# Kernel optimization log

Measured on AMD Instinct MI355X. Metric: run time of the kernel, lower is better.

## Reference

```python
import jax, jax.numpy as jnp
import numpy as np

V, E, H, D_IMG, A = 32000, 512, 512, 2048, 128
PAD_ID = 0
LN_EPS = 1e-5


def setup_inputs() -> dict:
    key = jax.random.key(0)
    ks = jax.random.split(key, 20)
    B, S, T = 32, 49, 64
    s = 0.02
    embed = jax.random.normal(ks[0], (V, E), jnp.float32) * s
    embed = embed.at[PAD_ID].set(0.0)
    return {
        "img_seq": jax.random.normal(ks[1], (B, S, D_IMG), jnp.float32),
        "tokens_in": jax.random.randint(ks[2], (B, T), 0, V, jnp.int64),
        "embed": embed,
        "W_ctx": jax.random.normal(ks[3], (E, D_IMG), jnp.float32) * s,
        "W_mix": jax.random.normal(ks[4], (E, 2 * E), jnp.float32) * s,
        "ln_g": jnp.ones((E,), jnp.float32),
        "ln_b": jnp.zeros((E,), jnp.float32),
        "W_ih": jax.random.normal(ks[5], (4 * H, E), jnp.float32) * s,
        "W_hh": jax.random.normal(ks[6], (4 * H, H), jnp.float32) * s,
        "b_ih": jnp.zeros((4 * H,), jnp.float32),
        "b_hh": jnp.zeros((4 * H,), jnp.float32),
        "W_head": jax.random.normal(ks[7], (V, H), jnp.float32) * s,
        "W_img": jax.random.normal(ks[8], (A, D_IMG), jnp.float32) * s,
        "W_hid": jax.random.normal(ks[9], (A, H), jnp.float32) * s,
        "w_score": jax.random.normal(ks[10], (A,), jnp.float32) * s,
        "W_h0": jax.random.normal(ks[11], (H, D_IMG), jnp.float32) * s,
        "b_h0": jnp.zeros((H,), jnp.float32),
        "W_c0": jax.random.normal(ks[12], (H, D_IMG), jnp.float32) * s,
        "b_c0": jnp.zeros((H,), jnp.float32),
    }


def _decode(img_seq, tokens_in, embed, W_ctx, W_mix, ln_g, ln_b,
            W_ih, W_hh, b_ih, b_hh, W_head, W_img, W_hid, w_score,
            W_h0, b_h0, W_c0, b_c0):
    # precompute image projection: [B,S,A]
    proj_image = jnp.einsum('bsd,ad->bsa', img_seq, W_img)
    g = img_seq.mean(1)  # [B, D_img]
    h = jnp.tanh(g @ W_h0.T + b_h0) * 0.5
    c = jnp.tanh(g @ W_c0.T + b_c0) * 0.5

    def step(carry, tok_t):
        h, c = carry
        emb = embed[tok_t] * (tok_t != PAD_ID)[:, None].astype(embed.dtype)
        # additive attention
        ph = h @ W_hid.T  # [B,A]
        comb = jnp.tanh(proj_image + ph[:, None, :])  # [B,S,A]
        scores = jnp.einsum('bsa,a->bs', comb, w_score)
        w = jax.nn.softmax(scores, axis=-1)
        ctx = jnp.einsum('bs,bsd->bd', w, img_seq)
        ctxE = ctx @ W_ctx.T
        x = jnp.concatenate([emb, ctxE], axis=-1) @ W_mix.T
        x = jax.nn.relu(x)
        mu = x.mean(-1, keepdims=True)
        var = ((x - mu) ** 2).mean(-1, keepdims=True)
        x = (x - mu) * jax.lax.rsqrt(var + LN_EPS) * ln_g + ln_b
        x = x + emb
        # LSTMCell (torch gate order: i, f, g, o)
        gates = x @ W_ih.T + b_ih + h @ W_hh.T + b_hh
        i_, f_, g_, o_ = jnp.split(gates, 4, axis=-1)
        c2 = jax.nn.sigmoid(f_) * c + jax.nn.sigmoid(i_) * jnp.tanh(g_)
        h2 = jax.nn.sigmoid(o_) * jnp.tanh(c2)
        logits = h2 @ W_head.T
        return (h2, c2), logits

    _, outs = jax.lax.scan(step, (h, c), tokens_in.T)  # [T,B,V]
    return jnp.transpose(outs, (1, 0, 2))  # [B,T,V]


def reference(img_seq, tokens_in, embed, W_ctx, W_mix, ln_g, ln_b,
              W_ih, W_hh, b_ih, b_hh, W_head, W_img, W_hid, w_score,
              W_h0, b_h0, W_c0, b_c0):
    return _decode(img_seq, tokens_in, embed, W_ctx, W_mix, ln_g, ln_b,
                   W_ih, W_hh, b_ih, b_hh, W_head, W_img, W_hid, w_score,
                   W_h0, b_h0, W_c0, b_c0)
```

## Files before the change

### kernel.cpp

```cpp
#include <hip/hip_runtime.h>

#define NV 32000
#define NT 64
#define NBLK 256u

typedef unsigned long long ull;
typedef unsigned short ushort;
typedef __attribute__((ext_vector_type(8))) short v8s;
typedef __attribute__((ext_vector_type(4))) float v4f;

#define WS_WBF     0
#define WS_H2BF    8192000
#define WS_IMGEM   8716288
#define WS_PROJ    9568256
#define WS_EMBM    9781248
#define WS_WHHBF   10829824
#define WS_WIHBF   11354112
#define WS_WHIDBF  11878400
#define WS_H       11911168
#define WS_XN      11943936
#define WS_C       11960320
#define WS_FLAGS   11976704
#define WS_G       11979264
#define PS_IMGBF   0
#define PS_WCTXBF  1703936
#define PS_WIMGBF  2228224
#define PS_WMIXRBF 2359296
#define PS_WMIXLBF 2490368
#define PS_IMGEBF  3342336

__device__ __forceinline__ float fsig(float x) {
    x = fminf(fmaxf(x, -30.f), 30.f);
    return 1.f / (1.f + __expf(-x));
}
__device__ __forceinline__ float ftanh(float x) {
    x = fminf(fmaxf(x, -15.f), 15.f);
    float e = __expf(2.f * x);
    return (e - 1.f) / (e + 1.f);
}
__device__ __forceinline__ unsigned short f2bf(float f) {
    union { float f; unsigned int u; } v; v.f = f;
    unsigned int u = v.u;
    return (unsigned short)((u + 0x7FFFu + ((u >> 16) & 1u)) >> 16);
}
__device__ __forceinline__ unsigned pkf(float x, float y) {
    return (unsigned)f2bf(x) | ((unsigned)f2bf(y) << 16);
}
__device__ __forceinline__ float bf_lo(unsigned u) { return __uint_as_float(u << 16); }
__device__ __forceinline__ float bf_hi(unsigned u) { return __uint_as_float(u & 0xffff0000u); }
__device__ __forceinline__ ull agld(const ull* p) {
    return __hip_atomic_load(p, __ATOMIC_RELAXED, __HIP_MEMORY_SCOPE_AGENT);
}
__device__ __forceinline__ unsigned pk2(ull v) {
    return (unsigned)f2bf(__uint_as_float((unsigned)v)) |
           ((unsigned)f2bf(__uint_as_float((unsigned)(v >> 32))) << 16);
}


__global__ __launch_bounds__(256) void k_castpad(const float* __restrict__ in,
        ushort* __restrict__ out, int R, int Rpad, int K, int ldi, int off) {
    size_t i = ((size_t)blockIdx.x * 256 + threadIdx.x) * 8;
    if (i >= (size_t)Rpad * K) return;
    int r = (int)(i / K), k = (int)(i % K);
    uint4 o = {0, 0, 0, 0};
    if (r < R) {
        const float* p = in + (size_t)r * ldi + off + k;
        float4 a = *(const float4*)(p);
        float4 b = *(const float4*)(p + 4);
        o.x = pkf(a.x, a.y); o.y = pkf(a.z, a.w);
        o.z = pkf(b.x, b.y); o.w = pkf(b.z, b.w);
    }
    *(uint4*)(out + i) = o;
}

__global__ __launch_bounds__(256) void k_castall(
        const float* __restrict__ img, const float* __restrict__ Wctx,
        const float* __restrict__ Wimg, const float* __restrict__ Wmix,
        const float* __restrict__ Whh, const float* __restrict__ Wih,
        const float* __restrict__ Whid,
        ushort* __restrict__ imgbf, ushort* __restrict__ wctxbf,
        ushort* __restrict__ wimgbf, ushort* __restrict__ wmixRbf,
        ushort* __restrict__ wmixLbf, ushort* __restrict__ whhbf,
        ushort* __restrict__ wihbf, ushort* __restrict__ whidbf,
        unsigned* __restrict__ flg) {
    int blk = blockIdx.x, tid = threadIdx.x;
    if (blk >= 3616) {
        for (int i = tid; i < 2560; i += 256) flg[i] = 0u;
        return;
    }
    const float* in; ushort* out; int R, K, ldi, off;
    if (blk < 1664)      { in = img;  out = imgbf;   R = 1568; K = 2048; ldi = 2048; off = 0; }
    else if (blk < 2176) { in = Wctx; out = wctxbf;  R = 512;  K = 2048; ldi = 2048; off = 0;   blk -= 1664; }
    else if (blk < 2304) { in = Wimg; out = wimgbf;  R = 128;  K = 2048; ldi = 2048; off = 0;   blk -= 2176; }
    else if (blk < 2432) { in = Wmix; out = wmixRbf; R = 512;  K = 512;  ldi = 1024; off = 512; blk -= 2304; }
    else if (blk < 2560) { in = Wmix; out = wmixLbf; R = 512;  K = 512;  ldi = 1024; off = 0;   blk -= 2432; }
    else if (blk < 3072) { in = Whh;  out = whhbf;   R = 2048; K = 512;  ldi = 512;  off = 0;   blk -= 2560; }
    else if (blk < 3584) { in = Wih;  out = wihbf;   R = 2048; K = 512;  ldi = 512;  off = 0;   blk -= 3072; }
    else                 { in = Whid; out = whidbf;  R = 128;  K = 512;  ldi = 512;  off = 0;   blk -= 3584; }
    size_t i = ((size_t)blk * 256 + tid) * 8;
    int r = (int)(i / K), k = (int)(i % K);
    uint4 o = {0, 0, 0, 0};
    if (r < R) {
        const float* p = in + (size_t)r * ldi + off + k;
        float4 a = *(const float4*)(p);
        float4 b = *(const float4*)(p + 4);
        o.x = pkf(a.x, a.y); o.y = pkf(a.z, a.w);
        o.z = pkf(b.x, b.y); o.w = pkf(b.z, b.w);
    }
    *(uint4*)(out + i) = o;
}

__global__ __launch_bounds__(256) void k_gemm(const ushort* __restrict__ A,
        const ushort* __restrict__ B, float* __restrict__ C, int N, int K) {
    __shared__ ushort Al[128][72];
    __shared__ ushort Bl[128][72];
    int n0 = blockIdx.x * 128, m0 = blockIdx.y * 128;
    int tid = threadIdx.x, lane = tid & 63, wid = tid >> 6;
    int wm = wid >> 1, wn = wid & 1;
    v4f acc[4][4] = {};
    for (int kt = 0; kt < K; kt += 64) {
        __syncthreads();
        #pragma unroll
        for (int i = 0; i < 4; i++) {
            int idx = i * 256 + tid;
            int row = idx >> 3, c8 = (idx & 7) * 8;
            *(uint4*)&Al[row][c8] = *(const uint4*)&A[(size_t)(m0 + row) * K + kt + c8];
            *(uint4*)&Bl[row][c8] = *(const uint4*)&B[(size_t)(n0 + row) * K + kt + c8];
        }
        __syncthreads();
        #pragma unroll
        for (int kk = 0; kk < 2; kk++) {
            v8s a[4], bfr[4];
            int ko = kk * 32 + (lane >> 4) * 8;
            #pragma unroll
            for (int mi = 0; mi < 4; mi++)
                a[mi] = *(const v8s*)&Al[wm * 64 + mi * 16 + (lane & 15)][ko];
            #pragma unroll
            for (int ni = 0; ni < 4; ni++)
                bfr[ni] = *(const v8s*)&Bl[wn * 64 + ni * 16 + (lane & 15)][ko];
            #pragma unroll
            for (int mi = 0; mi < 4; mi++)
                #pragma unroll
                for (int ni = 0; ni < 4; ni++)
                    acc[mi][ni] = __builtin_amdgcn_mfma_f32_16x16x32_bf16(a[mi], bfr[ni], acc[mi][ni], 0, 0, 0);
        }
    }
    int col = lane & 15, rbase = (lane >> 4) * 4;
    #pragma unroll
    for (int mi = 0; mi < 4; mi++)
        #pragma unroll
        for (int ni = 0; ni < 4; ni++)
            #pragma unroll
            for (int r = 0; r < 4; r++) {
                int m = m0 + wm * 64 + mi * 16 + rbase + r;
                int v = n0 + wn * 64 + ni * 16 + col;
                C[(size_t)m * N + v] = acc[mi][ni][r];
            }
}

__global__ __launch_bounds__(256) void k_gemm3(
        const ushort* __restrict__ imgbf, const ushort* __restrict__ wctxbf,
        const ushort* __restrict__ wimgbf, const float* __restrict__ embed,
        const int* __restrict__ toks, const ushort* __restrict__ wmixLbf,
        ushort* __restrict__ imgEbf, float* __restrict__ proj,
        float* __restrict__ embM) {
    __shared__ ushort Al[128][72];
    __shared__ ushort Bl[128][72];
    int bid = blockIdx.x;
    const ushort* A; const ushort* B; int mode, K, N, n0, m0;
    if (bid < 52)      { mode = 0; A = imgbf; B = wctxbf;  K = 2048; N = 512; n0 = (bid & 3) * 128; m0 = (bid >> 2) * 128; }
    else if (bid < 65) { mode = 1; A = imgbf; B = wimgbf;  K = 2048; N = 128; n0 = 0;               m0 = (bid - 52) * 128; }
    else { int e = bid - 65; mode = 2; A = nullptr; B = wmixLbf; K = 512; N = 512; n0 = (e & 3) * 128; m0 = (e >> 2) * 128; }
    int tid = threadIdx.x, lane = tid & 63, wid = tid >> 6;
    int wm = wid >> 1, wn = wid & 1;
    v4f acc[4][4] = {};
    for (int kt = 0; kt < K; kt += 64) {
        __syncthreads();
        #pragma unroll
        for (int i = 0; i < 4; i++) {
            int idx = i * 256 + tid;
            int row = idx >> 3, c8 = (idx & 7) * 8;
            if (mode == 2) {
                int rowg = m0 + row;
                int tok = toks[(rowg & 31) * 64 + (rowg >> 5)];
                uint4 oa = {0, 0, 0, 0};
                if (tok != 0) {
                    const float* pa = embed + (size_t)tok * 512 + kt + c8;
                    float4 a0 = *(const float4*)pa, a1 = *(const float4*)(pa + 4);
                    oa.x = pkf(a0.x, a0.y); oa.y = pkf(a0.z, a0.w);
                    oa.z = pkf(a1.x, a1.y); oa.w = pkf(a1.z, a1.w);
                }
                *(uint4*)&Al[row][c8] = oa;
            } else {
                *(uint4*)&Al[row][c8] = *(const uint4*)&A[(size_t)(m0 + row) * K + kt + c8];
            }
            *(uint4*)&Bl[row][c8] = *(const uint4*)&B[(size_t)(n0 + row) * K + kt + c8];
        }
        __syncthreads();
        #pragma unroll
        for (int kk = 0; kk < 2; kk++) {
            v8s a[4], bfr[4];
            int ko = kk * 32 + (lane >> 4) * 8;
            #pragma unroll
            for (int mi = 0; mi < 4; mi++)
                a[mi] = *(const v8s*)&Al[wm * 64 + mi * 16 + (lane & 15)][ko];
            #pragma unroll
            for (int ni = 0; ni < 4; ni++)
                bfr[ni] = *(const v8s*)&Bl[wn * 64 + ni * 16 + (lane & 15)][ko];
            #pragma unroll
            for (int mi = 0; mi < 4; mi++)
                #pragma unroll
                for (int ni = 0; ni < 4; ni++)
                    acc[mi][ni] = __builtin_amdgcn_mfma_f32_16x16x32_bf16(a[mi], bfr[ni], acc[mi][ni], 0, 0, 0);
        }
    }
    int col = lane & 15, rbase = (lane >> 4) * 4;
    #pragma unroll
    for (int mi = 0; mi < 4; mi++)
        #pragma unroll
        for (int ni = 0; ni < 4; ni++)
            #pragma unroll
            for (int r = 0; r < 4; r++) {
                int m = m0 + wm * 64 + mi * 16 + rbase + r;
                int v = n0 + wn * 64 + ni * 16 + col;
                if (mode == 0)      imgEbf[(size_t)m * 512 + v] = f2bf(acc[mi][ni][r]);
                else if (mode == 1) proj[(size_t)m * 128 + v] = acc[mi][ni][r];
                else                embM[(size_t)m * 512 + v] = acc[mi][ni][r];
            }
}

__global__ __launch_bounds__(256) void k_gmean(const float* __restrict__ img,
                                               float* __restrict__ g) {
    int b = blockIdx.x;
    for (int d = threadIdx.x; d < 2048; d += 256) {
        float s = 0.f;
        for (int ss = 0; ss < 49; ss++) s += img[((size_t)(b * 49 + ss)) * 2048 + d];
        g[b * 2048 + d] = s * (1.f / 49.f);
    }
}

__global__ __launch_bounds__(256) void k_h0c0(const float* __restrict__ g,
        const float* __restrict__ Wh0, const float* __restrict__ bh0,
        const float* __restrict__ Wc0, const float* __restrict__ bc0,
        float* __restrict__ h0, float* __restrict__ c0) {
    int b = blockIdx.x >> 1, m = blockIdx.x & 1;
    __shared__ float gs[2048];
    for (int d = threadIdx.x; d < 2048; d += 256) gs[d] = g[b * 2048 + d];
    __syncthreads();
    const float* W = m ? Wc0 : Wh0;
    const float* bb = m ? bc0 : bh0;
    float* out = m ? c0 : h0;
    for (int r = threadIdx.x; r < 512; r += 256) {
        float acc = 0.f;
        const float* wr = W + (size_t)r * 2048;
        for (int d = 0; d < 2048; d += 4) {
            float4 w = *(const float4*)(wr + d);
            acc += w.x * gs[d] + w.y * gs[d + 1] + w.z * gs[d + 2] + w.w * gs[d + 3];
        }
        out[b * 512 + r] = ftanh(acc + bb[r]) * 0.5f;
    }
}


__device__ __forceinline__ void waitflags(unsigned* FLG, int base, int stride,
                                          int n, unsigned tgt) {
    if (threadIdx.x < 64) {
        bool done;
        do {
            unsigned v = tgt;
            if ((int)threadIdx.x < n)
                v = __hip_atomic_load(FLG + (base + (int)threadIdx.x * stride) * 16,
                                      __ATOMIC_RELAXED, __HIP_MEMORY_SCOPE_AGENT);
            done = __all((int)(v >= tgt));
            if (!done) __builtin_amdgcn_s_sleep(1);
        } while (!done);
    }
    __syncthreads();
}

union SMem {
    struct {
        ushort wh[64][520];
        ushort wi[64][520];
        ushort hsb[16][520];
        float gtmp[4][16][16];
        ushort h2s[16][8];
    } g;
    struct {
        float imgem[49][512];
        float projl[49][128];
        float hb[512];
        float ebs[512];
        float php[8][128];
        float ph[128];
        float scp[64][16];
        float wsm[64];
        float xps[2][512];
        float wred[8][2];
        float bc[2];
    } a;
    struct {
        ushort Al[256][72];
        ushort Bl[128][72];
    } h;
};

__global__ __launch_bounds__(1024, 1) void k_persist(
        const int* __restrict__ toks, const float* __restrict__ embed,
        const float* __restrict__ lng, const float* __restrict__ lnb,
        const float* __restrict__ bih, const float* __restrict__ bhh,
        const float* __restrict__ wsc, const ushort* __restrict__ whidbf,
        const ushort* __restrict__ whhbf, const ushort* __restrict__ wihbf,
        const float* __restrict__ proj, const float* __restrict__ imgEM,
        const float* __restrict__ embM, float* __restrict__ H,
        const float* __restrict__ C0, float* __restrict__ XN,
        unsigned* __restrict__ FLG, ushort* __restrict__ h2bf,
        const ushort* __restrict__ Wbf, float* __restrict__ out) {
    __shared__ SMem sm;
    int blk = blockIdx.x, tid = threadIdx.x;

    if (blk < 128) {
        int jc = blk >> 2, bg = blk & 3, b0 = bg * 8;
        int wid = tid >> 6, lane = tid & 63;
        int gate = wid & 3;
        for (int i = tid; i < 4096; i += 1024) {
            int rr = i >> 6, c8 = (i & 63) * 8;
            size_t R = (size_t)((rr >> 4) * 512 + jc * 16 + (rr & 15)) * 512 + c8;
            *(uint4*)&sm.g.wh[rr][c8] = *(const uint4*)&whhbf[R];
            *(uint4*)&sm.g.wi[rr][c8] = *(const uint4*)&wihbf[R];
        }
        for (int i = tid; i < 2080; i += 1024) ((ull*)sm.g.hsb)[i] = 0;
        float c_reg = 0.f, bs0 = 0.f, bs1 = 0.f, bs2 = 0.f, bs3 = 0.f;
        if (tid < 128) {
            int jl = tid >> 3, bb = tid & 7;
            int j = jc * 16 + jl;
            c_reg = C0[(b0 + bb) * 512 + j];
            bs0 = bih[j] + bhh[j];
            bs1 = bih[512 + j] + bhh[512 + j];
            bs2 = bih[1024 + j] + bhh[1024 + j];
            bs3 = bih[1536 + j] + bhh[1536 + j];
        }
        __syncthreads();

        for (int t = 0; t < NT; t++) {
            waitflags(FLG, bg, 4, 32, (unsigned)t);
            {
                const float* Hb = H + (t & 1) * 16384 + b0 * 512;
                if (tid < 512) {
                    int bb = tid >> 6, c8 = (tid & 63) * 8;
                    const ull* p = (const ull*)(Hb + bb * 512 + c8);
                    uint4 o = { pk2(agld(p)), pk2(agld(p + 1)),
                                pk2(agld(p + 2)), pk2(agld(p + 3)) };
                    *(uint4*)&sm.g.hsb[bb][c8] = o;
                }
            }
            __syncthreads();
            v4f acc = {};
            if (wid < 4) {
                #pragma unroll
                for (int ks = 0; ks < 16; ks++) {
                    int ko = ks * 32 + (lane >> 4) * 8;
                    v8s a = *(const v8s*)&sm.g.hsb[lane & 15][ko];
                    v8s b = *(const v8s*)&sm.g.wh[gate * 16 + (lane & 15)][ko];
                    acc = __builtin_amdgcn_mfma_f32_16x16x32_bf16(a, b, acc, 0, 0, 0);
                }
            }
            waitflags(FLG, 128 + b0, 1, 8, (unsigned)(t + 1));
            {
                const float* Xb = XN + b0 * 512;
                if (tid < 512) {
                    int bb = tid >> 6, c8 = (tid & 63) * 8;
                    const ull* p = (const ull*)(Xb + bb * 512 + c8);
                    uint4 o = { pk2(agld(p)), pk2(agld(p + 1)),
                                pk2(agld(p + 2)), pk2(agld(p + 3)) };
                    *(uint4*)&sm.g.hsb[bb][c8] = o;
                }
            }
            __syncthreads();
            if (wid < 4) {
                #pragma unroll
                for (int ks = 0; ks < 16; ks++) {
                    int ko = ks * 32 + (lane >> 4) * 8;
                    v8s a = *(const v8s*)&sm.g.hsb[lane & 15][ko];
                    v8s b = *(const v8s*)&sm.g.wi[gate * 16 + (lane & 15)][ko];
                    acc = __builtin_amdgcn_mfma_f32_16x16x32_bf16(a, b, acc, 0, 0, 0);
                }
                #pragma unroll
                for (int q = 0; q < 4; q++)
                    sm.g.gtmp[gate][lane & 15][(lane >> 4) * 4 + q] = acc[q];
            }
            __syncthreads();
            if (tid < 128) {
                int jl = tid >> 3, bb = tid & 7;
                float vi = sm.g.gtmp[0][jl][bb] + bs0;
                float vf = sm.g.gtmp[1][jl][bb] + bs1;
                float vg = sm.g.gtmp[2][jl][bb] + bs2;
                float vo = sm.g.gtmp[3][jl][bb] + bs3;
                float c2 = fsig(vf) * c_reg + fsig(vi) * ftanh(vg);
                float h2 = fsig(vo) * ftanh(c2);
                c_reg = c2;
                int bglob = b0 + bb, j = jc * 16 + jl;
                __hip_atomic_store((unsigned*)&H[((t + 1) & 1) * 16384 + bglob * 512 + j],
                                   __float_as_uint(h2), __ATOMIC_RELAXED, __HIP_MEMORY_SCOPE_AGENT);
                sm.g.h2s[jl][bb] = f2bf(h2);
            }
            __syncthreads();
            if (tid < 64) {
                int jlp = tid >> 3, bb = tid & 7;
                unsigned pk = (unsigned)sm.g.h2s[2 * jlp][bb]
                            | ((unsigned)sm.g.h2s[2 * jlp + 1][bb] << 16);
                int bglob = b0 + bb, j = jc * 16 + 2 * jlp;
                __hip_atomic_store((unsigned*)&h2bf[(size_t)(t * 32 + bglob) * 512 + j],
                                   pk, __ATOMIC_RELAXED, __HIP_MEMORY_SCOPE_AGENT);
            }
            __syncthreads();
            if (tid == 0)
                __hip_atomic_store(FLG + blk * 16, (unsigned)(t + 1),
                                   __ATOMIC_RELAXED, __HIP_MEMORY_SCOPE_AGENT);
        }
    } else if (blk < 160) {
        int b = blk - 128, bgb = b >> 3;
        for (int i = tid; i < 49 * 512; i += 1024)
            sm.a.imgem[i >> 9][i & 511] = imgEM[(size_t)b * 49 * 512 + i];
        for (int i = tid; i < 49 * 128; i += 1024)
            sm.a.projl[i >> 7][i & 127] = proj[(size_t)b * 49 * 128 + i];
        __syncthreads();
        for (int t = 0; t < NT; t++) {
            waitflags(FLG, bgb, 4, 32, (unsigned)t);
            int tok = toks[b * 64 + t];
            if (tid < 256) {
                ull v = agld((const ull*)(H + (t & 1) * 16384) + b * 256 + tid);
                *(ull*)&sm.a.hb[tid * 2] = v;
            } else if (tid < 768) {
                int k = tid - 256;
                sm.a.ebs[k] = (tok == 0) ? 0.f : embed[(size_t)tok * 512 + k];
            }
            __syncthreads();
            {
                int a = tid & 127, kq = tid >> 7;
                const ushort* wr2 = whidbf + (size_t)a * 512 + kq * 64;
                const float* hp = sm.a.hb + kq * 64;
                float p = 0.f;
                #pragma unroll
                for (int k = 0; k < 64; k += 8) {
                    uint4 q = *(const uint4*)(wr2 + k);
                    float4 ha = *(const float4*)(hp + k);
                    float4 hb4 = *(const float4*)(hp + k + 4);
                    p += bf_lo(q.x)*ha.x + bf_hi(q.x)*ha.y + bf_lo(q.y)*ha.z + bf_hi(q.y)*ha.w
                       + bf_lo(q.z)*hb4.x + bf_hi(q.z)*hb4.y + bf_lo(q.w)*hb4.z + bf_hi(q.w)*hb4.w;
                }
                sm.a.php[kq][a] = p;
            }
            __syncthreads();
            if (tid < 128) {
                float p = 0.f;
                #pragma unroll
                for (int kq = 0; kq < 8; kq++) p += sm.a.php[kq][tid];
                sm.a.ph[tid] = p;
            }
            __syncthreads();
            {
                int s = tid >> 4, aq = tid & 15;
                float p = 0.f;
                if (s < 49) {
                    const float* pr = &sm.a.projl[s][aq * 8];
                    #pragma unroll
                    for (int a = 0; a < 8; a++)
                        p += ftanh(pr[a] + sm.a.ph[aq * 8 + a]) * wsc[aq * 8 + a];
                }
                sm.a.scp[s][aq] = p;
            }
            __syncthreads();
            if (tid < 64) {
                float v = 0.f;
                #pragma unroll
                for (int q = 0; q < 16; q++) v += sm.a.scp[tid][q];
                if (tid >= 49) v = -1e30f;
                float m = v;
                for (int o = 32; o > 0; o >>= 1) m = fmaxf(m, __shfl_xor(m, o));
                float e = (tid < 49) ? __expf(v - m) : 0.f;
                float su = e;
                for (int o = 32; o > 0; o >>= 1) su += __shfl_xor(su, o);
                sm.a.wsm[tid] = e / su;
            }
            __syncthreads();
            {
                int e = tid & 511, sh = tid >> 9;
                float xp = 0.f;
                if (sh == 0) xp = embM[(size_t)(t * 32 + b) * 512 + e];
                int s0 = sh * 25, s1 = sh ? 49 : 25;
                for (int s = s0; s < s1; s++)
                    xp += sm.a.wsm[s] * sm.a.imgem[s][e];
                sm.a.xps[sh][e] = xp;
            }
            __syncthreads();
            if (tid < 512) {
                float x = fmaxf(sm.a.xps[0][tid] + sm.a.xps[1][tid], 0.f);
                float s = x, s2 = x * x;
                for (int o = 32; o > 0; o >>= 1) { s += __shfl_xor(s, o); s2 += __shfl_xor(s2, o); }
                if ((tid & 63) == 0) { sm.a.wred[tid >> 6][0] = s; sm.a.wred[tid >> 6][1] = s2; }
            }
            __syncthreads();
            if (tid == 0) {
                float s = 0.f, s2 = 0.f;
                #pragma unroll
                for (int w = 0; w < 8; w++) { s += sm.a.wred[w][0]; s2 += sm.a.wred[w][1]; }
                float mu = s * (1.f / 512.f);
                float var = s2 * (1.f / 512.f) - mu * mu;
                sm.a.bc[0] = mu; sm.a.bc[1] = rsqrtf(var + 1e-5f);
            }
            __syncthreads();
            if (tid < 512) {
                float x = fmaxf(sm.a.xps[0][tid] + sm.a.xps[1][tid], 0.f);
                float xn = (x - sm.a.bc[0]) * sm.a.bc[1] * lng[tid] + lnb[tid] + sm.a.ebs[tid];
                __hip_atomic_store((unsigned*)&XN[b * 512 + tid], __float_as_uint(xn),
                                   __ATOMIC_RELAXED, __HIP_MEMORY_SCOPE_AGENT);
            }
            __syncthreads();
            if (tid == 0)
                __hip_atomic_store(FLG + (128 + b) * 16, (unsigned)(t + 1),
                                   __ATOMIC_RELAXED, __HIP_MEMORY_SCOPE_AGENT);
        }
    } else {
        int hb = blk - 160;
        int lane = tid & 63, wid = tid >> 6;
        int wm = wid >> 1, wn = wid & 1;
        unsigned have = 0;
        for (int w = hb; w < 2000; w += 96) {
            int mt = w / 250, nt = w % 250;
            unsigned need = (unsigned)(mt * 8 + 8);
            if (have < need) {
                if (tid < 64) {
                    bool done;
                    do {
                        unsigned v0 = __hip_atomic_load(FLG + tid * 16,
                                        __ATOMIC_RELAXED, __HIP_MEMORY_SCOPE_AGENT);
                        unsigned v1 = __hip_atomic_load(FLG + (tid + 64) * 16,
                                        __ATOMIC_RELAXED, __HIP_MEMORY_SCOPE_AGENT);
                        done = __all((int)(v0 >= need && v1 >= need));
                        if (!done) __builtin_amdgcn_s_sleep(8);
                    } while (!done);
                }
                __syncthreads();
                have = need;
            }
            int m0 = mt * 256, n0 = nt * 128;
            v4f acc[4][4] = {};
            for (int kt = 0; kt < 512; kt += 64) {
                __syncthreads();
                #pragma unroll
                for (int i = 0; i < 2; i++) {
                    int idx = i * 1024 + tid;
                    int row = idx >> 3, c8 = (idx & 7) * 8;
                    const ull* p = (const ull*)&h2bf[(size_t)(m0 + row) * 512 + kt + c8];
                    ull v0 = agld(p), v1 = agld(p + 1);
                    *(ull*)&sm.h.Al[row][c8] = v0;
                    *(ull*)&sm.h.Al[row][c8 + 4] = v1;
                }
                {
                    int row = tid >> 3, c8 = (tid & 7) * 8;
                    *(uint4*)&sm.h.Bl[row][c8] = *(const uint4*)&Wbf[(size_t)(n0 + row) * 512 + kt + c8];
                }
                __syncthreads();
                if (wid < 8) {
                    #pragma unroll
                    for (int kk = 0; kk < 2; kk++) {
                        v8s a[4], bfr[4];
                        int ko = kk * 32 + (lane >> 4) * 8;
                        #pragma unroll
                        for (int mi = 0; mi < 4; mi++)
                            a[mi] = *(const v8s*)&sm.h.Al[wm * 64 + mi * 16 + (lane & 15)][ko];
                        #pragma unroll
                        for (int ni = 0; ni < 4; ni++)
                            bfr[ni] = *(const v8s*)&sm.h.Bl[wn * 64 + ni * 16 + (lane & 15)][ko];
                        #pragma unroll
                        for (int mi = 0; mi < 4; mi++)
                            #pragma unroll
                            for (int ni = 0; ni < 4; ni++)
                                acc[mi][ni] = __builtin_amdgcn_mfma_f32_16x16x32_bf16(a[mi], bfr[ni], acc[mi][ni], 0, 0, 0);
                    }
                }
            }
            if (wid < 8) {
                int col = lane & 15, rbase = (lane >> 4) * 4;
                #pragma unroll
                for (int mi = 0; mi < 4; mi++)
                    #pragma unroll
                    for (int ni = 0; ni < 4; ni++)
                        #pragma unroll
                        for (int r = 0; r < 4; r++) {
                            int m = m0 + wm * 64 + mi * 16 + rbase + r;
                            int v = n0 + wn * 64 + ni * 16 + col;
                            int b = m & 31, t = m >> 5;
                            out[((size_t)(b * 64 + t)) * 32000 + v] = acc[mi][ni][r];
                        }
            }
        }
    }
}

extern "C" void kernel_launch(void* const* d_in, const int* in_sizes, int n_in,
                              void* d_out, int out_size, void* d_ws, size_t ws_size,
                              hipStream_t stream) {
    const float* img    = (const float*)d_in[0];
    const int*   toks   = (const int*)d_in[1];
    const float* embed  = (const float*)d_in[2];
    const float* W_ctx  = (const float*)d_in[3];
    const float* W_mix  = (const float*)d_in[4];
    const float* ln_g   = (const float*)d_in[5];
    const float* ln_b   = (const float*)d_in[6];
    const float* W_ih   = (const float*)d_in[7];
    const float* W_hh   = (const float*)d_in[8];
    const float* b_ih   = (const float*)d_in[9];
    const float* b_hh   = (const float*)d_in[10];
    const float* W_head = (const float*)d_in[11];
    const float* W_img  = (const float*)d_in[12];
    const float* W_hid  = (const float*)d_in[13];
    const float* w_sc   = (const float*)d_in[14];
    const float* W_h0   = (const float*)d_in[15];
    const float* b_h0   = (const float*)d_in[16];
    const float* W_c0   = (const float*)d_in[17];
    const float* b_c0   = (const float*)d_in[18];

    float* out = (float*)d_out;
    float* ws  = (float*)d_ws;
    ushort* Wbf    = (ushort*)(ws + WS_WBF);
    ushort* h2bf   = (ushort*)(ws + WS_H2BF);
    float*  imgEM  = ws + WS_IMGEM;
    float*  proj   = ws + WS_PROJ;
    float*  embM   = ws + WS_EMBM;
    ushort* whhbf  = (ushort*)(ws + WS_WHHBF);
    ushort* wihbf  = (ushort*)(ws + WS_WIHBF);
    ushort* whidbf = (ushort*)(ws + WS_WHIDBF);
    float*  H      = ws + WS_H;
    float*  XN     = ws + WS_XN;
    float*  C      = ws + WS_C;
    unsigned* flg  = (unsigned*)(ws + WS_FLAGS);
    float*  g      = ws + WS_G;
    ushort* imgbf   = (ushort*)(ws + PS_IMGBF);
    ushort* wctxbf  = (ushort*)(ws + PS_WCTXBF);
    ushort* wimgbf  = (ushort*)(ws + PS_WIMGBF);
    ushort* wmixRbf = (ushort*)(ws + PS_WMIXRBF);
    ushort* wmixLbf = (ushort*)(ws + PS_WMIXLBF);
    ushort* imgEbf  = (ushort*)(ws + PS_IMGEBF);

    k_castall<<<3617, 256, 0, stream>>>(img, W_ctx, W_img, W_mix, W_hh, W_ih, W_hid,
                                        imgbf, wctxbf, wimgbf, wmixRbf, wmixLbf,
                                        whhbf, wihbf, whidbf, flg);
    k_gemm3<<<129, 256, 0, stream>>>(imgbf, wctxbf, wimgbf, embed, toks, wmixLbf,
                                     imgEbf, proj, embM);
    k_gemm<<<dim3(4, 13), 256, 0, stream>>>(imgEbf, wmixRbf, imgEM, 512, 512);
    k_castpad<<<8000, 256, 0, stream>>>(W_head, Wbf, 32000, 32000, 512, 512, 0);
    k_gmean<<<32, 256, 0, stream>>>(img, g);
    k_h0c0<<<64, 256, 0, stream>>>(g, W_h0, b_h0, W_c0, b_c0, H, C);

    k_persist<<<NBLK, 1024, 0, stream>>>(toks, embed, ln_g, ln_b, b_ih, b_hh, w_sc,
                                         whidbf, whhbf, wihbf, proj, imgEM, embM,
                                         H, C, XN, flg, h2bf, Wbf, out);
}
```

Measured before the change: 1.007 ms.

## Distribute final head row-tile across all blocks via atomic work counter

The dedicated head blocks now handle only the first seven row-tiles of the output projection. The last row-tile, which depends on the final decode steps, is shared by every block, including the recurrence and attention blocks once they finish. Those blocks take column tiles dynamically through an atomic counter in the flag buffer. This is meant to shorten the tail after the recurrence finishes, at the cost of a counter slot in FLG that must start at zero.

```diff
diff --git a/kernel.cpp b/kernel.cpp
--- a/kernel.cpp
+++ b/kernel.cpp
@@ -273,6 +273,22 @@
                                       __ATOMIC_RELAXED, __HIP_MEMORY_SCOPE_AGENT);
             done = __all((int)(v >= tgt));
             if (!done) __builtin_amdgcn_s_sleep(1);
+        } while (!done);
+    }
+    __syncthreads();
+}
+
+template <int SLP>
+__device__ __forceinline__ void waitgates(unsigned* FLG, unsigned tgt) {
+    if (threadIdx.x < 64) {
+        bool done;
+        do {
+            unsigned v0 = __hip_atomic_load(FLG + threadIdx.x * 16,
+                            __ATOMIC_RELAXED, __HIP_MEMORY_SCOPE_AGENT);
+            unsigned v1 = __hip_atomic_load(FLG + (threadIdx.x + 64) * 16,
+                            __ATOMIC_RELAXED, __HIP_MEMORY_SCOPE_AGENT);
+            done = __all((int)(v0 >= tgt && v1 >= tgt));
+            if (!done) __builtin_amdgcn_s_sleep(SLP);
         } while (!done);
     }
     __syncthreads();
@@ -305,6 +321,62 @@
     } h;
 };
 
+__device__ __forceinline__ void head_tile(SMem& sm, const ushort* __restrict__ h2bf,
+        const ushort* __restrict__ Wbf, float* __restrict__ out, int m0, int n0) {
+    int tid = threadIdx.x, lane = tid & 63, wid = tid >> 6;
+    int wm = wid >> 1, wn = wid & 1;
+    v4f acc[4][4] = {};
+    for (int kt = 0; kt < 512; kt += 64) {
+        __syncthreads();
+        #pragma unroll
+        for (int i = 0; i < 2; i++) {
+            int idx = i * 1024 + tid;
+            int row = idx >> 3, c8 = (idx & 7) * 8;
+            const ull* p = (const ull*)&h2bf[(size_t)(m0 + row) * 512 + kt + c8];
+            ull v0 = agld(p), v1 = agld(p + 1);
+            *(ull*)&sm.h.Al[row][c8] = v0;
+            *(ull*)&sm.h.Al[row][c8 + 4] = v1;
+        }
+        {
+            int row = tid >> 3, c8 = (tid & 7) * 8;
+            *(uint4*)&sm.h.Bl[row][c8] = *(const uint4*)&Wbf[(size_t)(n0 + row) * 512 + kt + c8];
+        }
+        __syncthreads();
+        if (wid < 8) {
+            #pragma unroll
+            for (int kk = 0; kk < 2; kk++) {
+                v8s a[4], bfr[4];
+                int ko = kk * 32 + (lane >> 4) * 8;
+                #pragma unroll
+                for (int mi = 0; mi < 4; mi++)
+                    a[mi] = *(const v8s*)&sm.h.Al[wm * 64 + mi * 16 + (lane & 15)][ko];
+                #pragma unroll
+                for (int ni = 0; ni < 4; ni++)
+                    bfr[ni] = *(const v8s*)&sm.h.Bl[wn * 64 + ni * 16 + (lane & 15)][ko];
+                #pragma unroll
+                for (int mi = 0; mi < 4; mi++)
+                    #pragma unroll
+                    for (int ni = 0; ni < 4; ni++)
+                        acc[mi][ni] = __builtin_amdgcn_mfma_f32_16x16x32_bf16(a[mi], bfr[ni], acc[mi][ni], 0, 0, 0);
+            }
+        }
+    }
+    if (wid < 8) {
+        int col = lane & 15, rbase = (lane >> 4) * 4;
+        #pragma unroll
+        for (int mi = 0; mi < 4; mi++)
+            #pragma unroll
+            for (int ni = 0; ni < 4; ni++)
+                #pragma unroll
+                for (int r = 0; r < 4; r++) {
+                    int m = m0 + wm * 64 + mi * 16 + rbase + r;
+                    int v = n0 + wn * 64 + ni * 16 + col;
+                    int b = m & 31, t = m >> 5;
+                    out[((size_t)(b * 64 + t)) * 32000 + v] = acc[mi][ni][r];
+                }
+    }
+}
+
 __global__ __launch_bounds__(1024, 1) void k_persist(
         const int* __restrict__ toks, const float* __restrict__ embed,
         const float* __restrict__ lng, const float* __restrict__ lnb,
@@ -317,6 +389,7 @@
         unsigned* __restrict__ FLG, ushort* __restrict__ h2bf,
         const ushort* __restrict__ Wbf, float* __restrict__ out) {
     __shared__ SMem sm;
+    __shared__ unsigned sh_w;
     int blk = blockIdx.x, tid = threadIdx.x;
 
     if (blk < 128) {
@@ -523,79 +596,25 @@
         }
     } else {
         int hb = blk - 160;
-        int lane = tid & 63, wid = tid >> 6;
-        int wm = wid >> 1, wn = wid & 1;
         unsigned have = 0;
-        for (int w = hb; w < 2000; w += 96) {
+        for (int w = hb; w < 1750; w += 96) {
             int mt = w / 250, nt = w % 250;
             unsigned need = (unsigned)(mt * 8 + 8);
-            if (have < need) {
-                if (tid < 64) {
-                    bool done;
-                    do {
-                        unsigned v0 = __hip_atomic_load(FLG + tid * 16,
-                                        __ATOMIC_RELAXED, __HIP_MEMORY_SCOPE_AGENT);
-                        unsigned v1 = __hip_atomic_load(FLG + (tid + 64) * 16,
-                                        __ATOMIC_RELAXED, __HIP_MEMORY_SCOPE_AGENT);
-                        done = __all((int)(v0 >= need && v1 >= need));
-                        if (!done) __builtin_amdgcn_s_sleep(8);
-                    } while (!done);
-                }
-                __syncthreads();
-                have = need;
-            }
-            int m0 = mt * 256, n0 = nt * 128;
-            v4f acc[4][4] = {};
-            for (int kt = 0; kt < 512; kt += 64) {
-                __syncthreads();
-                #pragma unroll
-                for (int i = 0; i < 2; i++) {
-                    int idx = i * 1024 + tid;
-                    int row = idx >> 3, c8 = (idx & 7) * 8;
-                    const ull* p = (const ull*)&h2bf[(size_t)(m0 + row) * 512 + kt + c8];
-                    ull v0 = agld(p), v1 = agld(p + 1);
-                    *(ull*)&sm.h.Al[row][c8] = v0;
-                    *(ull*)&sm.h.Al[row][c8 + 4] = v1;
-                }
-                {
-                    int row = tid >> 3, c8 = (tid & 7) * 8;
-                    *(uint4*)&sm.h.Bl[row][c8] = *(const uint4*)&Wbf[(size_t)(n0 + row) * 512 + kt + c8];
-                }
-                __syncthreads();
-                if (wid < 8) {
-                    #pragma unroll
-                    for (int kk = 0; kk < 2; kk++) {
-                        v8s a[4], bfr[4];
-                        int ko = kk * 32 + (lane >> 4) * 8;
-                        #pragma unroll
-                        for (int mi = 0; mi < 4; mi++)
-                            a[mi] = *(const v8s*)&sm.h.Al[wm * 64 + mi * 16 + (lane & 15)][ko];
-                        #pragma unroll
-                        for (int ni = 0; ni < 4; ni++)
-                            bfr[ni] = *(const v8s*)&sm.h.Bl[wn * 64 + ni * 16 + (lane & 15)][ko];
-                        #pragma unroll
-                        for (int mi = 0; mi < 4; mi++)
-                            #pragma unroll
-                            for (int ni = 0; ni < 4; ni++)
-                                acc[mi][ni] = __builtin_amdgcn_mfma_f32_16x16x32_bf16(a[mi], bfr[ni], acc[mi][ni], 0, 0, 0);
-                    }
-                }
-            }
-            if (wid < 8) {
-                int col = lane & 15, rbase = (lane >> 4) * 4;
-                #pragma unroll
-                for (int mi = 0; mi < 4; mi++)
-                    #pragma unroll
-                    for (int ni = 0; ni < 4; ni++)
-                        #pragma unroll
-                        for (int r = 0; r < 4; r++) {
-                            int m = m0 + wm * 64 + mi * 16 + rbase + r;
-                            int v = n0 + wn * 64 + ni * 16 + col;
-                            int b = m & 31, t = m >> 5;
-                            out[((size_t)(b * 64 + t)) * 32000 + v] = acc[mi][ni][r];
-                        }
-            }
-        }
+            if (have < need) { waitgates<8>(FLG, need); have = need; }
+            head_tile(sm, h2bf, Wbf, out, mt * 256, nt * 128);
+        }
+    }
+
+    waitgates<2>(FLG, (unsigned)NT);
+    for (;;) {
+        if (tid == 0)
+            sh_w = __hip_atomic_fetch_add(FLG + 8, 1u, __ATOMIC_RELAXED,
+                                          __HIP_MEMORY_SCOPE_AGENT);
+        __syncthreads();
+        unsigned w = sh_w;
+        __syncthreads();
+        if (w >= 250u) break;
+        head_tile(sm, h2bf, Wbf, out, 7 * 256, (int)w * 128);
     }
 }
 
```

New measurement: 983.3 us. -2.3%, faster.
